# Kernel optimization log

Measured on AMD Instinct MI355X. Metric: run time of the kernel, lower is better.

## Reference

```python
import jax, jax.numpy as jnp
import numpy as np

EMBED_DIM = 1024
NUM_HEADS = 16
HEAD_DIM = EMBED_DIM // NUM_HEADS


def setup_inputs() -> dict:
    key = jax.random.key(0)
    k_x, k_wqkv, k_bqkv, k_wo, k_bo = jax.random.split(key, 5)
    B, T, C = 8, 1024, EMBED_DIM
    s = 1.0 / np.sqrt(C)
    return {
        "x": jax.random.normal(k_x, (B, T, C), dtype=jnp.float32),
        "W_qkv": jax.random.uniform(k_wqkv, (C, 3 * C), minval=-s, maxval=s, dtype=jnp.float32),
        "b_qkv": jax.random.uniform(k_bqkv, (3 * C,), minval=-s, maxval=s, dtype=jnp.float32),
        "W_out": jax.random.uniform(k_wo, (C, C), minval=-s, maxval=s, dtype=jnp.float32),
        "b_out": jax.random.uniform(k_bo, (C,), minval=-s, maxval=s, dtype=jnp.float32),
    }


def reference(x, W_qkv, b_qkv, W_out, b_out):
    B, T, C = x.shape
    H, D = NUM_HEADS, HEAD_DIM
    qkv = x @ W_qkv + b_qkv                      # [B,T,3C]
    q, k, v = jnp.split(qkv, 3, axis=-1)
    q = q.reshape(B, T, H, D).transpose(0, 2, 1, 3)  # [B,H,T,D]
    k = k.reshape(B, T, H, D).transpose(0, 2, 1, 3)
    v = v.reshape(B, T, H, D).transpose(0, 2, 1, 3)
    scores = jnp.einsum("bhqd,bhkd->bhqk", q, k) / np.sqrt(D).astype(np.float32)
    causal = jnp.tril(jnp.ones((T, T), dtype=bool))
    scores = jnp.where(causal[None, None], scores, -jnp.inf)
    attn = jax.nn.softmax(scores, axis=-1)       # dropout is identity in eval
    out = jnp.einsum("bhqk,bhkd->bhqd", attn, v)
    out = out.transpose(0, 2, 1, 3).reshape(B, T, C)
    return out @ W_out + b_out
```

## Files before the change

### kernel.cpp

```cpp
#include <hip/hip_runtime.h>
#include <hip/hip_bf16.h>
#include <cstdint>

using bf16 = __hip_bfloat16;
typedef short short8 __attribute__((ext_vector_type(8)));
typedef float floatx4 __attribute__((ext_vector_type(4)));

#define QSCALE 0.1803368801111601f

__device__ __forceinline__ void async_load16(const bf16* g, bf16* l) {
    __builtin_amdgcn_global_load_lds(
        (const __attribute__((address_space(1))) uint32_t*)g,
        (__attribute__((address_space(3))) uint32_t*)l, 16, 0, 0);
}

__device__ __forceinline__ void bar_lgkm0() {
    asm volatile("s_waitcnt lgkmcnt(0)\ns_barrier" ::: "memory");
}
__device__ __forceinline__ void bar_vm4() {
    asm volatile("s_waitcnt vmcnt(4)\ns_barrier" ::: "memory");
}
__device__ __forceinline__ void bar_vm0() {
    asm volatile("s_waitcnt vmcnt(0)\ns_barrier" ::: "memory");
}
__device__ __forceinline__ void bar_vm4_lgkm0() {
    asm volatile("s_waitcnt vmcnt(4) lgkmcnt(0)\ns_barrier" ::: "memory");
}
__device__ __forceinline__ void bar_vm0_lgkm0() {
    asm volatile("s_waitcnt vmcnt(0) lgkmcnt(0)\ns_barrier" ::: "memory");
}

__device__ __forceinline__ uint32_t pack2(float a, float b) {
    union { bf16 h[2]; uint32_t u; } p;
    p.h[0] = __float2bfloat16(a);
    p.h[1] = __float2bfloat16(b);
    return p.u;
}

__global__ __launch_bounds__(256)
void cvt_bf16_kernel(const float* __restrict__ in, bf16* __restrict__ out) {
    const int i = (blockIdx.x * 256 + threadIdx.x) * 4;
    const float4 v = *(const float4*)(in + i);
    bf16 o[4] = {__float2bfloat16(v.x), __float2bfloat16(v.y),
                 __float2bfloat16(v.z), __float2bfloat16(v.w)};
    *(ushort4*)(out + i) = *(ushort4*)o;
}

__global__ __launch_bounds__(256)
void transpose_cvt2_kernel(const float* __restrict__ inA, bf16* __restrict__ outA,
                           const float* __restrict__ inB, bf16* __restrict__ outB) {
    __shared__ float tile[32][33];
    const int tx = threadIdx.x & 31, ty = threadIdx.x >> 5;
    const bool isB = blockIdx.x >= 96;
    const float* __restrict__ in = isB ? inB : inA;
    bf16* __restrict__ out = isB ? outB : outA;
    const int C = isB ? 1024 : 3072;
    const int bx = isB ? blockIdx.x - 96 : blockIdx.x;
    const int c0 = bx * 32, r0 = blockIdx.y * 32;
    const int R = 1024;
    #pragma unroll
    for (int i = 0; i < 32; i += 8)
        tile[ty + i][tx] = in[(size_t)(r0 + ty + i) * C + c0 + tx];
    __syncthreads();
    #pragma unroll
    for (int i = 0; i < 32; i += 8)
        out[(size_t)(c0 + ty + i) * R + r0 + tx] = __float2bfloat16(tile[tx][ty + i]);
}

template <int MODE>
__global__ __launch_bounds__(256, 3)
void gemm_bt_kernel(const bf16* __restrict__ A, const bf16* __restrict__ Bt,
                    const float* __restrict__ bias, int K,
                    bf16* __restrict__ q_ws, bf16* __restrict__ k_ws,
                    bf16* __restrict__ vt_ws, float* __restrict__ out, int N) {
    __shared__ bf16 As[3][128 * 32];
    __shared__ bf16 Bs[3][128 * 32];
    const int tid = threadIdx.x;
    const int wave = tid >> 6, lane = tid & 63;
    const int ln = lane & 15, quad = lane >> 4;
    const int wm = wave & 1, wn = wave >> 1;
    const int m0 = blockIdx.y * 128, n0 = blockIdx.x * 128;

    floatx4 acc[4][4] = {};
    const int nkt = K >> 5;

    #pragma unroll
    for (int t = 0; t < 2; ++t) {
        const int k0 = t << 5;
        #pragma unroll
        for (int c = 0; c < 2; ++c) {
            const int e = (c * 256 + tid) * 8;
            const int row = e >> 5;
            const int gch = ((((e >> 3) & 3) ^ ((row >> 1) & 3)) << 3);
            async_load16(A + (size_t)(m0 + row) * K + k0 + gch,
                         &As[t][(c * 256 + wave * 64) * 8]);
        }
        #pragma unroll
        for (int c = 0; c < 2; ++c) {
            const int e = (c * 256 + tid) * 8;
            const int row = e >> 5;
            const int gch = ((((e >> 3) & 3) ^ ((row >> 1) & 3)) << 3);
            async_load16(Bt + (size_t)(n0 + row) * K + k0 + gch,
                         &Bs[t][(c * 256 + wave * 64) * 8]);
        }
    }

    for (int kt = 0; kt < nkt; ++kt) {
        const int cur = kt % 3;
        if (kt + 1 < nkt) bar_vm4_lgkm0();
        else              bar_vm0_lgkm0();

        if (kt + 2 < nkt) {
            const int nxt = (kt + 2) % 3;
            const int k0 = (kt + 2) << 5;
            #pragma unroll
            for (int c = 0; c < 2; ++c) {
                const int e = (c * 256 + tid) * 8;
                const int row = e >> 5;
                const int gch = ((((e >> 3) & 3) ^ ((row >> 1) & 3)) << 3);
                async_load16(A + (size_t)(m0 + row) * K + k0 + gch,
                             &As[nxt][(c * 256 + wave * 64) * 8]);
            }
            #pragma unroll
            for (int c = 0; c < 2; ++c) {
                const int e = (c * 256 + tid) * 8;
                const int row = e >> 5;
                const int gch = ((((e >> 3) & 3) ^ ((row >> 1) & 3)) << 3);
                async_load16(Bt + (size_t)(n0 + row) * K + k0 + gch,
                             &Bs[nxt][(c * 256 + wave * 64) * 8]);
            }
        }

        const int chq = ((quad ^ ((ln >> 1) & 3)) << 3);
        short8 af[4], bfr[4];
        #pragma unroll
        for (int i = 0; i < 4; ++i) {
            af[i]  = *(const short8*)&As[cur][(wm * 64 + i * 16 + ln) * 32 + chq];
            bfr[i] = *(const short8*)&Bs[cur][(wn * 64 + i * 16 + ln) * 32 + chq];
        }
        #pragma unroll
        for (int mi = 0; mi < 4; ++mi)
            #pragma unroll
            for (int ni = 0; ni < 4; ++ni)
                acc[mi][ni] = __builtin_amdgcn_mfma_f32_16x16x32_bf16(
                    af[mi], bfr[ni], acc[mi][ni], 0, 0, 0);
    }

    #pragma unroll
    for (int ni = 0; ni < 4; ++ni) {
        const int col = n0 + wn * 64 + ni * 16 + ln;
        const float bv = bias[col];
        if (MODE == 0) {
            const int which = col >> 10;
            const int cc = col & 1023;
            const int h = cc >> 6, d = cc & 63;
            #pragma unroll
            for (int mi = 0; mi < 4; ++mi) {
                const int rowb = m0 + wm * 64 + mi * 16 + quad * 4;
                if (which == 2) {
                    const int bb = rowb >> 10, t = rowb & 1023;
                    const int tl = t & 63;
                    const int tt = (t & ~63) + ((((tl >> 3) ^ (d & 7)) << 3) | (tl & 7));
                    uint2 w2 = { pack2(acc[mi][ni][0] + bv, acc[mi][ni][1] + bv),
                                 pack2(acc[mi][ni][2] + bv, acc[mi][ni][3] + bv) };
                    *(uint2*)&vt_ws[((size_t)(bb * 16 + h) * 64 + d) * 1024 + tt] = w2;
                } else {
                    bf16* dst = (which == 0) ? q_ws : k_ws;
                    #pragma unroll
                    for (int r = 0; r < 4; ++r) {
                        const int row = rowb + r;
                        const int bb = row >> 10, t = row & 1023;
                        float v = acc[mi][ni][r] + bv;
                        if (which == 0) v *= QSCALE;
                        const int dd = (((d >> 3) ^ (t & 7)) << 3) | (d & 7);
                        dst[((size_t)(bb * 16 + h) * 1024 + t) * 64 + dd] =
                            __float2bfloat16(v);
                    }
                }
            }
        } else {
            #pragma unroll
            for (int mi = 0; mi < 4; ++mi) {
                const int rowb = m0 + wm * 64 + mi * 16 + quad * 4;
                #pragma unroll
                for (int r = 0; r < 4; ++r)
                    out[(size_t)(rowb + r) * N + col] = acc[mi][ni][r] + bv;
            }
        }
    }
}

__global__ __launch_bounds__(256, 3)
void attn_kernel(const bf16* __restrict__ Q, const bf16* __restrict__ K,
                 const bf16* __restrict__ Vt, bf16* __restrict__ O) {
    constexpr int T = 1024;
    __shared__ bf16 QPs[128 * 64];
    __shared__ bf16 Ks[2][64 * 64];
    __shared__ bf16 Vts[2][64 * 64];

    const int bh = blockIdx.y;
    const int tid = threadIdx.x;
    const int wave = tid >> 6, lane = tid & 63;
    const int ln = lane & 15, quad = lane >> 4;

    const bf16* Kg = K + (size_t)bh * T * 64;
    const bf16* Vg = Vt + (size_t)bh * 64 * T;
    const int b = bh >> 4, h = bh & 15;

    const int jt = 7 - blockIdx.x;
    const int q0 = jt * 128;
    const int nkt = 2 * jt + 2;

    const bf16* Qg = Q + (size_t)bh * T * 64 + (size_t)q0 * 64;
    #pragma unroll
    for (int c = 0; c < 4; ++c)
        async_load16(Qg + (size_t)(c * 256 + tid) * 8,
                     &QPs[(c * 256 + wave * 64) * 8]);
    #pragma unroll
    for (int c = 0; c < 2; ++c)
        async_load16(Kg + (size_t)(c * 256 + tid) * 8,
                     &Ks[0][(c * 256 + wave * 64) * 8]);
    #pragma unroll
    for (int c = 0; c < 2; ++c) {
        const int e = (c * 256 + tid) * 8;
        async_load16(Vg + (size_t)(e >> 6) * T + (e & 63),
                     &Vts[0][(c * 256 + wave * 64) * 8]);
    }
    bar_vm0();

    short8 bq[2][2];
    #pragma unroll
    for (int qs = 0; qs < 2; ++qs)
        #pragma unroll
        for (int ks = 0; ks < 2; ++ks) {
            const int row = wave * 16 + qs * 64 + ln;
            const int ch = (ks * 4 + quad) ^ (row & 7);
            bq[qs][ks] = *(const short8*)&QPs[row * 64 + ch * 8];
        }

    floatx4 oacc[2][4] = {};
    float rl[2] = {0.f, 0.f};
    const int qb0 = q0 + wave * 16;
    const int qb1 = qb0 + 64;

    for (int kt = 0; kt < nkt; ++kt) {
        const int cur = kt & 1;
        bar_lgkm0();
        if (kt + 1 < nkt) {
            const int nxt = cur ^ 1;
            #pragma unroll
            for (int c = 0; c < 2; ++c)
                async_load16(Kg + (size_t)(kt + 1) * 4096 + (size_t)(c * 256 + tid) * 8,
                             &Ks[nxt][(c * 256 + wave * 64) * 8]);
            #pragma unroll
            for (int c = 0; c < 2; ++c) {
                const int e = (c * 256 + tid) * 8;
                async_load16(Vg + (size_t)(e >> 6) * T + (kt + 1) * 64 + (e & 63),
                             &Vts[nxt][(c * 256 + wave * 64) * 8]);
            }
            bar_vm4();
        } else {
            bar_vm0();
        }

        const int k0 = kt * 64;
        if (k0 > qb1 + 15) continue;
        const bool tail = (k0 + 63 > qb0);

        floatx4 sacc[2][4] = {};
        __builtin_amdgcn_s_setprio(1);
        #pragma unroll
        for (int nj = 0; nj < 4; ++nj) {
            short8 ak[2];
            #pragma unroll
            for (int ks = 0; ks < 2; ++ks) {
                const int row = nj * 16 + ln;
                const int ch = (ks * 4 + quad) ^ (row & 7);
                ak[ks] = *(const short8*)&Ks[cur][row * 64 + ch * 8];
            }
            #pragma unroll
            for (int qs = 0; qs < 2; ++qs) {
                const int qb = qs ? qb1 : qb0;
                if (k0 + nj * 16 > qb + 15) continue;
                #pragma unroll
                for (int ks = 0; ks < 2; ++ks)
                    sacc[qs][nj] = __builtin_amdgcn_mfma_f32_16x16x32_bf16(
                        ak[ks], bq[qs][ks], sacc[qs][nj], 0, 0, 0);
            }
        }
        __builtin_amdgcn_s_setprio(0);

        if (tail) {
            #pragma unroll
            for (int qs = 0; qs < 2; ++qs) {
                const int qq = (qs ? qb1 : qb0) + ln;
                #pragma unroll
                for (int nj = 0; nj < 4; ++nj)
                    #pragma unroll
                    for (int r = 0; r < 4; ++r) {
                        const int kk = k0 + nj * 16 + quad * 4 + r;
                        if (kk > qq) sacc[qs][nj][r] = -1e30f;
                    }
            }
        }

        #pragma unroll
        for (int qs = 0; qs < 2; ++qs) {
            float rs = 0.f;
            const int qrow = wave * 16 + qs * 64 + ln;
            #pragma unroll
            for (int nj = 0; nj < 4; ++nj) {
                float p[4];
                #pragma unroll
                for (int r = 0; r < 4; ++r) {
                    p[r] = exp2f(sacc[qs][nj][r]);
                    rs += p[r];
                }
                const int kcol = nj * 16 + quad * 4;
                const int ch = (kcol >> 3) ^ (qrow & 7);
                uint2 w2 = { pack2(p[0], p[1]), pack2(p[2], p[3]) };
                *(uint2*)&QPs[qrow * 64 + ch * 8 + (kcol & 7)] = w2;
            }
            rl[qs] += rs;
        }

        __builtin_amdgcn_s_setprio(1);
        #pragma unroll
        for (int ks4 = 0; ks4 < 2; ++ks4) {
            short8 bp[2];
            #pragma unroll
            for (int qs = 0; qs < 2; ++qs) {
                const int qrow = wave * 16 + qs * 64 + ln;
                const int chp = (ks4 * 4 + quad) ^ (qrow & 7);
                bp[qs] = *(const short8*)&QPs[qrow * 64 + chp * 8];
            }
            #pragma unroll
            for (int dt = 0; dt < 4; ++dt) {
                const int row = dt * 16 + ln;
                const int ch = (ks4 * 4 + quad) ^ (row & 7);
                const short8 av = *(const short8*)&Vts[cur][row * 64 + ch * 8];
                #pragma unroll
                for (int qs = 0; qs < 2; ++qs)
                    oacc[qs][dt] = __builtin_amdgcn_mfma_f32_16x16x32_bf16(
                        av, bp[qs], oacc[qs][dt], 0, 0, 0);
            }
        }
        __builtin_amdgcn_s_setprio(0);
    }

    #pragma unroll
    for (int qs = 0; qs < 2; ++qs) {
        float l = rl[qs];
        l += __shfl_xor(l, 16, 64);
        l += __shfl_xor(l, 32, 64);
        const float inv = 1.0f / l;
        const int t = q0 + qs * 64 + wave * 16 + ln;
        const size_t rowb = ((size_t)b * 1024 + t) * 1024 + h * 64;
        #pragma unroll
        for (int dt = 0; dt < 4; ++dt) {
            uint2 w2 = { pack2(oacc[qs][dt][0] * inv, oacc[qs][dt][1] * inv),
                         pack2(oacc[qs][dt][2] * inv, oacc[qs][dt][3] * inv) };
            *(uint2*)&O[rowb + dt * 16 + quad * 4] = w2;
        }
    }
}

extern "C" void kernel_launch(void* const* d_in, const int* in_sizes, int n_in,
                              void* d_out, int out_size, void* d_ws, size_t ws_size,
                              hipStream_t stream) {
    const float* x     = (const float*)d_in[0];
    const float* W_qkv = (const float*)d_in[1];
    const float* b_qkv = (const float*)d_in[2];
    const float* W_out = (const float*)d_in[3];
    const float* b_out = (const float*)d_in[4];
    float* out = (float*)d_out;

    char* ws = (char*)d_ws;
    const size_t MB = 1u << 20;
    bf16* x_bf   = (bf16*)(ws + 0);
    bf16* wqkv_t = (bf16*)(ws + 16 * MB);
    bf16* wout_t = (bf16*)(ws + 22 * MB);
    bf16* q_ws   = (bf16*)(ws + 24 * MB);
    bf16* k_ws   = (bf16*)(ws + 40 * MB);
    bf16* vt_ws  = (bf16*)(ws + 56 * MB);
    bf16* ao_ws  = (bf16*)(ws + 72 * MB);

    cvt_bf16_kernel<<<8192, 256, 0, stream>>>(x, x_bf);
    transpose_cvt2_kernel<<<dim3(128, 32), 256, 0, stream>>>(W_qkv, wqkv_t, W_out, wout_t);

    gemm_bt_kernel<0><<<dim3(24, 64), 256, 0, stream>>>(
        x_bf, wqkv_t, b_qkv, 1024, q_ws, k_ws, vt_ws, nullptr, 3072);

    attn_kernel<<<dim3(8, 128), 256, 0, stream>>>(q_ws, k_ws, vt_ws, ao_ws);

    gemm_bt_kernel<1><<<dim3(8, 64), 256, 0, stream>>>(
        ao_ws, wout_t, b_out, 1024, nullptr, nullptr, nullptr, out, 1024);
}
```

Baseline: 267.5 us.

## Read K/V directly from global memory in attention, drop LDS staging

The attention kernel stops staging Q, K and V tiles in shared memory with double-buffered async loads and barriers. Each wave now reads its MFMA operands straight from global memory and runs its own causal trip count, while LDS holds only the P tile. The block index is also remapped so heads of one batch group together for L2 locality, and exp2f is replaced by the raw v_exp_f32 instruction. This removes block barriers and LDS traffic but relies on L2/L1 to absorb the repeated, strided global reads, especially the column-strided Vt loads.

After: 239.5 us. 10.5% less time.

```diff
diff --git a/kernel.cpp b/kernel.cpp
--- a/kernel.cpp
+++ b/kernel.cpp
@@ -14,15 +14,6 @@
         (__attribute__((address_space(3))) uint32_t*)l, 16, 0, 0);
 }
 
-__device__ __forceinline__ void bar_lgkm0() {
-    asm volatile("s_waitcnt lgkmcnt(0)\ns_barrier" ::: "memory");
-}
-__device__ __forceinline__ void bar_vm4() {
-    asm volatile("s_waitcnt vmcnt(4)\ns_barrier" ::: "memory");
-}
-__device__ __forceinline__ void bar_vm0() {
-    asm volatile("s_waitcnt vmcnt(0)\ns_barrier" ::: "memory");
-}
 __device__ __forceinline__ void bar_vm4_lgkm0() {
     asm volatile("s_waitcnt vmcnt(4) lgkmcnt(0)\ns_barrier" ::: "memory");
 }
@@ -35,6 +26,12 @@
     p.h[0] = __float2bfloat16(a);
     p.h[1] = __float2bfloat16(b);
     return p.u;
+}
+
+__device__ __forceinline__ float fast_exp2(float x) {
+    float r;
+    asm("v_exp_f32 %0, %1" : "=v"(r) : "v"(x));
+    return r;
 }
 
 __global__ __launch_bounds__(256)
@@ -194,39 +191,21 @@
 void attn_kernel(const bf16* __restrict__ Q, const bf16* __restrict__ K,
                  const bf16* __restrict__ Vt, bf16* __restrict__ O) {
     constexpr int T = 1024;
-    __shared__ bf16 QPs[128 * 64];
-    __shared__ bf16 Ks[2][64 * 64];
-    __shared__ bf16 Vts[2][64 * 64];
-
-    const int bh = blockIdx.y;
+    __shared__ bf16 Ps[128 * 64];
+
+    const int lid = blockIdx.x + (blockIdx.y << 3);
+    const int bh = ((lid & 7) << 4) | ((lid >> 3) & 15);
+    const int jt = 7 - (lid >> 7);
+    const int q0 = jt << 7;
+
     const int tid = threadIdx.x;
     const int wave = tid >> 6, lane = tid & 63;
     const int ln = lane & 15, quad = lane >> 4;
-
+    const int b = bh >> 4, h = bh & 15;
+
+    const bf16* Qg = Q + ((size_t)bh * T + q0) * 64;
     const bf16* Kg = K + (size_t)bh * T * 64;
     const bf16* Vg = Vt + (size_t)bh * 64 * T;
-    const int b = bh >> 4, h = bh & 15;
-
-    const int jt = 7 - blockIdx.x;
-    const int q0 = jt * 128;
-    const int nkt = 2 * jt + 2;
-
-    const bf16* Qg = Q + (size_t)bh * T * 64 + (size_t)q0 * 64;
-    #pragma unroll
-    for (int c = 0; c < 4; ++c)
-        async_load16(Qg + (size_t)(c * 256 + tid) * 8,
-                     &QPs[(c * 256 + wave * 64) * 8]);
-    #pragma unroll
-    for (int c = 0; c < 2; ++c)
-        async_load16(Kg + (size_t)(c * 256 + tid) * 8,
-                     &Ks[0][(c * 256 + wave * 64) * 8]);
-    #pragma unroll
-    for (int c = 0; c < 2; ++c) {
-        const int e = (c * 256 + tid) * 8;
-        async_load16(Vg + (size_t)(e >> 6) * T + (e & 63),
-                     &Vts[0][(c * 256 + wave * 64) * 8]);
-    }
-    bar_vm0();
 
     short8 bq[2][2];
     #pragma unroll
@@ -234,37 +213,18 @@
         #pragma unroll
         for (int ks = 0; ks < 2; ++ks) {
             const int row = wave * 16 + qs * 64 + ln;
-            const int ch = (ks * 4 + quad) ^ (row & 7);
-            bq[qs][ks] = *(const short8*)&QPs[row * 64 + ch * 8];
+            const int ch = (ks * 4 + quad) ^ (ln & 7);
+            bq[qs][ks] = *(const short8*)(Qg + (size_t)row * 64 + ch * 8);
         }
 
     floatx4 oacc[2][4] = {};
     float rl[2] = {0.f, 0.f};
     const int qb0 = q0 + wave * 16;
     const int qb1 = qb0 + 64;
-
-    for (int kt = 0; kt < nkt; ++kt) {
-        const int cur = kt & 1;
-        bar_lgkm0();
-        if (kt + 1 < nkt) {
-            const int nxt = cur ^ 1;
-            #pragma unroll
-            for (int c = 0; c < 2; ++c)
-                async_load16(Kg + (size_t)(kt + 1) * 4096 + (size_t)(c * 256 + tid) * 8,
-                             &Ks[nxt][(c * 256 + wave * 64) * 8]);
-            #pragma unroll
-            for (int c = 0; c < 2; ++c) {
-                const int e = (c * 256 + tid) * 8;
-                async_load16(Vg + (size_t)(e >> 6) * T + (kt + 1) * 64 + (e & 63),
-                             &Vts[nxt][(c * 256 + wave * 64) * 8]);
-            }
-            bar_vm4();
-        } else {
-            bar_vm0();
-        }
-
-        const int k0 = kt * 64;
-        if (k0 > qb1 + 15) continue;
+    const int nktw = ((qb1 + 15) >> 6) + 1;
+
+    for (int kt = 0; kt < nktw; ++kt) {
+        const int k0 = kt << 6;
         const bool tail = (k0 + 63 > qb0);
 
         floatx4 sacc[2][4] = {};
@@ -274,9 +234,9 @@
             short8 ak[2];
             #pragma unroll
             for (int ks = 0; ks < 2; ++ks) {
-                const int row = nj * 16 + ln;
-                const int ch = (ks * 4 + quad) ^ (row & 7);
-                ak[ks] = *(const short8*)&Ks[cur][row * 64 + ch * 8];
+                const int trow = k0 + nj * 16 + ln;
+                const int ch = (ks * 4 + quad) ^ (ln & 7);
+                ak[ks] = *(const short8*)(Kg + (size_t)trow * 64 + ch * 8);
             }
             #pragma unroll
             for (int qs = 0; qs < 2; ++qs) {
@@ -313,13 +273,13 @@
                 float p[4];
                 #pragma unroll
                 for (int r = 0; r < 4; ++r) {
-                    p[r] = exp2f(sacc[qs][nj][r]);
+                    p[r] = fast_exp2(sacc[qs][nj][r]);
                     rs += p[r];
                 }
                 const int kcol = nj * 16 + quad * 4;
                 const int ch = (kcol >> 3) ^ (qrow & 7);
                 uint2 w2 = { pack2(p[0], p[1]), pack2(p[2], p[3]) };
-                *(uint2*)&QPs[qrow * 64 + ch * 8 + (kcol & 7)] = w2;
+                *(uint2*)&Ps[qrow * 64 + ch * 8 + (kcol & 7)] = w2;
             }
             rl[qs] += rs;
         }
@@ -331,14 +291,14 @@
             #pragma unroll
             for (int qs = 0; qs < 2; ++qs) {
                 const int qrow = wave * 16 + qs * 64 + ln;
-                const int chp = (ks4 * 4 + quad) ^ (qrow & 7);
-                bp[qs] = *(const short8*)&QPs[qrow * 64 + chp * 8];
+                const int chp = (ks4 * 4 + quad) ^ (ln & 7);
+                bp[qs] = *(const short8*)&Ps[qrow * 64 + chp * 8];
             }
             #pragma unroll
             for (int dt = 0; dt < 4; ++dt) {
-                const int row = dt * 16 + ln;
-                const int ch = (ks4 * 4 + quad) ^ (row & 7);
-                const short8 av = *(const short8*)&Vts[cur][row * 64 + ch * 8];
+                const int d = dt * 16 + ln;
+                const int ch = (ks4 * 4 + quad) ^ (ln & 7);
+                const short8 av = *(const short8*)(Vg + (size_t)d * T + k0 + ch * 8);
                 #pragma unroll
                 for (int qs = 0; qs < 2; ++qs)
                     oacc[qs][dt] = __builtin_amdgcn_mfma_f32_16x16x32_bf16(
```
